# Kernel tuning notes

Measured on AMD Instinct MI355X. Metric: run time of the kernel, lower is better.

## Reference

```python
import jax, jax.numpy as jnp
import numpy as np

N, F, T, C = 20000, 4, 12, 256
HID, OUT = 128, 12
ER, E = 30000, 320000


def _gcn_agg(xw, src, dst, w):
    """GCNConv propagation with self-loops (weight 1): D^-1/2 (A+I) D^-1/2 @ xw.
    xw: [N, T, C] pre-projected features; src/dst: [E] int; w: [E] edge weights."""
    n = xw.shape[0]
    deg = jnp.zeros((n,), xw.dtype).at[dst].add(w) + 1.0  # +1 from self-loop
    dinv = jax.lax.rsqrt(deg)
    coef = (dinv[src] * w * dinv[dst])[:, None, None]      # [E,1,1]
    out = jnp.zeros_like(xw).at[dst].add(coef * xw[src])   # scatter-add messages
    return out + (dinv * dinv)[:, None, None] * xw         # self-loop term


def _regional_conv(x, Wc, bc, regs):
    # Shared GCNConv applied to each of the 5 state graphs, outputs summed.
    xw = jnp.einsum("nft,fc->ntc", x, Wc)  # [N, T, C], all periods at once
    out = bc
    for (src, dst, w) in regs:
        out = out + _gcn_agg(xw, src, dst, w)
    return out


def _forward(x, attrs, idxs, Wc_z, bc_z, Wl_z, bl_z, Wc_h, bc_h, Wl_h, bl_h,
             attention, W1, b1, W2, b2):
    regs = [(idx[0], idx[1], w) for idx, w in zip(idxs, attrs)]
    # A3TGCN runs an independent TGCN-GRU step per period from H=None (zeros),
    # then attention-averages over periods. With H=0:
    #   Z = sigmoid(linear_z([conv_z(X_t), 0]))   (hidden half of Wl drops out)
    #   reset gate R multiplies H=0, so it has no effect on the output
    #   H_tilde = tanh(linear_h([conv_h(X_t), 0]));  H_t = (1-Z)*H_tilde
    cz = _regional_conv(x, Wc_z, bc_z, regs)         # [N, T, C]
    Z = jax.nn.sigmoid(cz @ Wl_z[:C] + bl_z)
    ch = _regional_conv(x, Wc_h, bc_h, regs)
    Htilde = jnp.tanh(ch @ Wl_h[:C] + bl_h)
    Ht = (1.0 - Z) * Htilde                          # [N, T, C]
    probs = jax.nn.softmax(attention)                # [T]
    h = jnp.einsum("ntc,t->nc", Ht, probs)           # temporal attention pooling
    y = jax.nn.relu(h)
    y = jax.nn.relu(y @ W1 + b1)
    y = y @ W2 + b2
    return y, h


def setup_inputs():
    key = jax.random.key(0)
    ks = jax.random.split(key, 32)
    s = 0.05
    inp = {
        "x": jax.random.normal(ks[0], (N, F, T), jnp.float32),
        "edge_index": jax.random.randint(ks[1], (2, E), 0, N, jnp.int32),
    }
    regions = ["IA", "KS", "KY", "OH", "WI"]
    for i, nm in enumerate(regions):
        inp[nm + "edge_index"] = jax.random.randint(ks[2 + i], (2, ER), 0, N, jnp.int32)
    for i, nm in enumerate(regions):
        inp[nm + "edge_attr"] = jax.random.uniform(ks[7 + i], (ER,), jnp.float32)
    for gi, g in enumerate(["z", "r", "h"]):
        inp["Wc_" + g] = jax.random.normal(ks[12 + gi], (F, C), jnp.float32) * s
        inp["bc_" + g] = jnp.zeros((C,), jnp.float32)
        inp["Wl_" + g] = jax.random.normal(ks[15 + gi], (2 * C, C), jnp.float32) * s
        inp["bl_" + g] = jnp.zeros((C,), jnp.float32)
    inp["attention"] = jax.random.normal(ks[18], (T,), jnp.float32)
    inp["W1"] = jax.random.normal(ks[19], (C, HID), jnp.float32) * s
    inp["b1"] = jnp.zeros((HID,), jnp.float32)
    inp["W2"] = jax.random.normal(ks[20], (HID, OUT), jnp.float32) * s
    inp["b2"] = jnp.zeros((OUT,), jnp.float32)
    return inp


def reference(x, edge_index, IAedge_index, KSedge_index, KYedge_index, OHedge_index, WIedge_index,
              IAedge_attr, KSedge_attr, KYedge_attr, OHedge_attr, WIedge_attr,
              Wc_z, bc_z, Wl_z, bl_z, Wc_r, bc_r, Wl_r, bl_r, Wc_h, bc_h, Wl_h, bl_h,
              attention, W1, b1, W2, b2):
    # The full-graph edge_index and the reset-gate parameters are carried by the
    # original module but cannot influence the output (regional convs use the 5
    # state graphs; the reset gate multiplies the zero initial hidden state).
    idxs = [IAedge_index, KSedge_index, KYedge_index, OHedge_index, WIedge_index]
    attrs = [IAedge_attr, KSedge_attr, KYedge_attr, OHedge_attr, WIedge_attr]
    return _forward(x, attrs, idxs, Wc_z, bc_z, Wl_z, bl_z, Wc_h, bc_h, Wl_h, bl_h,
                    attention, W1, b1, W2, b2)
```

## Files before the change

### kernel.cpp

```cpp
#include <hip/hip_runtime.h>

constexpr int N    = 20000;
constexpr int T    = 12;
constexpr int C    = 256;
constexpr int HIDN = 128;
constexpr int OUTD = 12;
constexpr int ER   = 30000;
constexpr int NFT  = 48;
constexpr int EDGE_TOT = 5 * ER;
constexpr int CAP      = 32;
constexpr int EB       = 586;

constexpr int WS_DEG    = 0;
constexpr int WS_CNT    = 100000;
constexpr int WS_MV     = 120000;
constexpr int WS_ZEND   = 122576;
constexpr int WS_WP     = 122576;
constexpr int WS_W2T    = 138960;
constexpr int WS_XV     = 140496;
constexpr int WS_BUCKET = 1100496;

constexpr float LOG2E = 1.4426950408889634f;

typedef __attribute__((ext_vector_type(8))) short short8;
typedef __attribute__((ext_vector_type(4))) float floatx4;

#if __has_builtin(__builtin_amdgcn_exp2f)
#define EXP2(x) __builtin_amdgcn_exp2f(x)
#else
#define EXP2(x) exp2f(x)
#endif

__device__ __forceinline__ short f2bf(float f) {
  unsigned u = __float_as_uint(f);
  u = u + 0x7fffu + ((u >> 16) & 1u);
  return (short)(u >> 16);
}

__device__ __forceinline__ void pick_region(
    int r,
    const int* e0, const int* e1, const int* e2, const int* e3, const int* e4,
    const float* a0, const float* a1, const float* a2, const float* a3, const float* a4,
    const int*& ei, const float*& ea) {
  switch (r) {
    case 0: ei = e0; ea = a0; break;
    case 1: ei = e1; ea = a1; break;
    case 2: ei = e2; ea = a2; break;
    case 3: ei = e3; ea = a3; break;
    default: ei = e4; ea = a4; break;
  }
}

__global__ void k_prep_deg(
    const float* __restrict__ Wc_z, const float* __restrict__ bc_z,
    const float* __restrict__ Wl_z, const float* __restrict__ bl_z,
    const float* __restrict__ Wc_h, const float* __restrict__ bc_h,
    const float* __restrict__ Wl_h, const float* __restrict__ bl_h,
    const float* __restrict__ att, const float* __restrict__ W1,
    const float* __restrict__ W2,
    const int* __restrict__ e0, const int* __restrict__ e1,
    const int* __restrict__ e2, const int* __restrict__ e3,
    const int* __restrict__ e4,
    const float* __restrict__ a0, const float* __restrict__ a1,
    const float* __restrict__ a2, const float* __restrict__ a3,
    const float* __restrict__ a4,
    float* __restrict__ Mv, short* __restrict__ Wp, float* __restrict__ W2t,
    float* __restrict__ deg) {
  int b = blockIdx.x, tid = threadIdx.x;
  if (b < 16) {
    int g  = b >> 3;
    int ch = b & 7;
    int k  = tid;
    const float* Wc = g ? Wc_h : Wc_z;
    const float* bc = g ? bc_h : bc_z;
    const float* Wl = g ? Wl_h : Wl_z;
    const float* bl = g ? bl_h : bl_z;
    float scale = g ? 2.0f * LOG2E : LOG2E;
    float m0 = 0.f, m1 = 0.f, m2 = 0.f, m3 = 0.f;
    float v = (ch == 0) ? bl[k] : 0.0f;
    int c0 = ch * 32;
    for (int c = c0; c < c0 + 32; c++) {
      float wl = Wl[c * C + k];
      m0 = fmaf(Wc[0 * C + c], wl, m0);
      m1 = fmaf(Wc[1 * C + c], wl, m1);
      m2 = fmaf(Wc[2 * C + c], wl, m2);
      m3 = fmaf(Wc[3 * C + c], wl, m3);
      v  = fmaf(bc[c], wl, v);
    }
    float* o = Mv + g * (5 * C);
    atomicAdd(&o[0 * C + k], scale * m0);
    atomicAdd(&o[1 * C + k], scale * m1);
    atomicAdd(&o[2 * C + k], scale * m2);
    atomicAdd(&o[3 * C + k], scale * m3);
    atomicAdd(&o[4 * C + k], scale * v);
    return;
  }
  if (b == 16) {
    if (tid < T) {
      float amax = -3.0e38f;
      for (int t = 0; t < T; t++) amax = fmaxf(amax, att[t]);
      float s = 0.f;
      for (int t = 0; t < T; t++) s += __expf(att[t] - amax);
      Mv[10 * C + tid] = __expf(att[tid] - amax) / s;
    }
    return;
  }
  if (b < 152) {
    int idx = (b - 17) * 256 + tid;
    if (idx < 32768) {
      int j    = idx & 7;
      int lane = (idx >> 3) & 63;
      int ch   = (idx >> 9) & 7;
      int kt   = idx >> 12;
      int cin  = ch * 32 + (lane >> 4) * 8 + j;
      int kout = kt * 16 + (lane & 15);
      Wp[idx] = f2bf(W1[cin * HIDN + kout]);
    } else if (idx < 32768 + 1536) {
      int r = idx - 32768;
      int o = r >> 7, k = r & 127;
      W2t[r] = W2[k * OUTD + o];
    }
    return;
  }
  int i = (b - 152) * 256 + tid;
  if (i >= EDGE_TOT) return;
  int r = i / ER;
  int e = i - r * ER;
  const int* ei; const float* ea;
  pick_region(r, e0, e1, e2, e3, e4, a0, a1, a2, a3, a4, ei, ea);
  atomicAdd(&deg[r * N + ei[ER + e]], ea[e]);
}

__global__ void k_fill(const int* __restrict__ e0, const int* __restrict__ e1,
                       const int* __restrict__ e2, const int* __restrict__ e3,
                       const int* __restrict__ e4,
                       const float* __restrict__ a0, const float* __restrict__ a1,
                       const float* __restrict__ a2, const float* __restrict__ a3,
                       const float* __restrict__ a4,
                       const float* __restrict__ deg, int* __restrict__ cnt,
                       int2* __restrict__ bucket) {
  int i = blockIdx.x * blockDim.x + threadIdx.x;
  if (i >= EDGE_TOT) return;
  int r = i / ER;
  int e = i - r * ER;
  const int* ei; const float* ea;
  pick_region(r, e0, e1, e2, e3, e4, a0, a1, a2, a3, a4, ei, ea);
  int src = ei[e];
  int dst = ei[ER + e];
  float cf = rsqrtf(deg[r * N + src] + 1.0f) * ea[e] * rsqrtf(deg[r * N + dst] + 1.0f);
  int slot = atomicAdd(&cnt[dst], 1);
  if (slot < CAP) bucket[dst * CAP + slot] = make_int2(src, __float_as_int(cf));
}

__global__ __launch_bounds__(256) void k_gather(
    const float* __restrict__ x, const float* __restrict__ deg,
    const int* __restrict__ cnt, const int2* __restrict__ bucket,
    float* __restrict__ xv) {
  int wave = threadIdx.x >> 6, lane = threadIdx.x & 63;
  int n = blockIdx.x * 4 + wave;
  int q = lane < NFT ? lane : NFT - 1;
  float s = 0.f;
#pragma unroll
  for (int r = 0; r < 5; r++) s += 1.0f / (deg[r * N + n] + 1.0f);
  float facc = s * x[n * NFT + q];
  int cv = cnt[n];
  if (cv > CAP) cv = CAP;
  int2 mreg = bucket[n * CAP + (lane & (CAP - 1))];
  for (int j = 0; j < cv; j++) {
    int   src = __shfl(mreg.x, j);
    float cf  = __int_as_float(__shfl(mreg.y, j));
    facc = fmaf(cf, x[src * NFT + q], facc);
  }
  if (lane < NFT) xv[n * NFT + q] = facc;
}

__global__ __launch_bounds__(256) void k_gates(
    const float* __restrict__ xv, const float* __restrict__ Mv,
    float* __restrict__ h_out) {
  int wave = threadIdx.x >> 6, lane = threadIdx.x & 63;
  int n = blockIdx.x * 2 + (wave >> 1);
  int half = wave & 1;
  int c0 = half * 128 + (lane << 1);
  const float* Mz = Mv;
  const float* Mh = Mv + 5 * C;
  float mz[4][2], mh[4][2], vz[2], vh[2];
#pragma unroll
  for (int f = 0; f < 4; f++) {
    float2 t1 = *(const float2*)(Mz + f * C + c0);
    mz[f][0] = t1.x; mz[f][1] = t1.y;
    float2 t2 = *(const float2*)(Mh + f * C + c0);
    mh[f][0] = t2.x; mh[f][1] = t2.y;
  }
  {
    float2 t1 = *(const float2*)(Mz + 4 * C + c0);
    vz[0] = t1.x; vz[1] = t1.y;
    float2 t2 = *(const float2*)(Mh + 4 * C + c0);
    vh[0] = t2.x; vh[1] = t2.y;
  }

  const float* xr = xv + n * NFT;
  float acc[2] = {0.f, 0.f};
#pragma unroll
  for (int tb = 0; tb < 3; tb++) {
    float4 xf0 = *(const float4*)(xr + 0 * T + tb * 4);
    float4 xf1 = *(const float4*)(xr + 1 * T + tb * 4);
    float4 xf2 = *(const float4*)(xr + 2 * T + tb * 4);
    float4 xf3 = *(const float4*)(xr + 3 * T + tb * 4);
    float xs0[4] = {xf0.x, xf0.y, xf0.z, xf0.w};
    float xs1[4] = {xf1.x, xf1.y, xf1.z, xf1.w};
    float xs2[4] = {xf2.x, xf2.y, xf2.z, xf2.w};
    float xs3[4] = {xf3.x, xf3.y, xf3.z, xf3.w};
#pragma unroll
    for (int tt = 0; tt < 4; tt++) {
      int t = tb * 4 + tt;
      float p = Mv[10 * C + t];
      float x0 = xs0[tt], x1 = xs1[tt], x2 = xs2[tt], x3 = xs3[tt];
#pragma unroll
      for (int j = 0; j < 2; j++) {
        float az = fmaf(mz[0][j], x0, fmaf(mz[1][j], x1, fmaf(mz[2][j], x2, fmaf(mz[3][j], x3, vz[j]))));
        float ah = fmaf(mh[0][j], x0, fmaf(mh[1][j], x1, fmaf(mh[2][j], x2, fmaf(mh[3][j], x3, vh[j]))));
        float e1 = EXP2(az);
        float e2 = EXP2(ah);
        float den = (1.0f + e1) * (1.0f + e2);
        float rD  = __builtin_amdgcn_rcpf(den);
        float pn  = fmaf(p, e2, -p);
        acc[j] = fmaf(pn, rD, acc[j]);
      }
    }
  }
  float2 o = {acc[0], acc[1]};
  *(float2*)(h_out + n * C + c0) = o;
}

__global__ __launch_bounds__(256) void k_mlp16(
    const float* __restrict__ h_in, const short* __restrict__ Wp,
    const float* __restrict__ b1, const float* __restrict__ W2t,
    const float* __restrict__ b2, float* __restrict__ y_out) {
  __shared__ short hs[16][264];
  __shared__ float y1s[16][132];
  int tid = threadIdx.x;
  int wave = tid >> 6, lane = tid & 63;
  int quad = lane >> 4, col = lane & 15;
  int n0 = blockIdx.x * 16;
  int c0 = lane << 2;

#pragma unroll
  for (int nl = 0; nl < 4; nl++) {
    int rl = wave * 4 + nl;
    float4 hv = *(const float4*)(h_in + (n0 + rl) * C + c0);
    unsigned lo = (unsigned short)f2bf(fmaxf(hv.x, 0.f)) |
                  ((unsigned)(unsigned short)f2bf(fmaxf(hv.y, 0.f)) << 16);
    unsigned hi = (unsigned short)f2bf(fmaxf(hv.z, 0.f)) |
                  ((unsigned)(unsigned short)f2bf(fmaxf(hv.w, 0.f)) << 16);
    *(int2*)&hs[rl][c0] = make_int2((int)lo, (int)hi);
  }
  __syncthreads();

  floatx4 acc2[2];
  acc2[0] = {0.f, 0.f, 0.f, 0.f};
  acc2[1] = {0.f, 0.f, 0.f, 0.f};
#pragma unroll
  for (int ch = 0; ch < 8; ch++) {
    short8 a = *(const short8*)&hs[col][ch * 32 + quad * 8];
#pragma unroll
    for (int kk = 0; kk < 2; kk++) {
      short8 b = ((const short8*)Wp)[((wave * 2 + kk) * 8 + ch) * 64 + lane];
      acc2[kk] = __builtin_amdgcn_mfma_f32_16x16x32_bf16(a, b, acc2[kk], 0, 0, 0);
    }
  }
#pragma unroll
  for (int kk = 0; kk < 2; kk++) {
    int kt = wave * 2 + kk;
    float bias = b1[kt * 16 + col];
#pragma unroll
    for (int r = 0; r < 4; r++)
      y1s[quad * 4 + r][kt * 16 + col] = fmaxf(acc2[kk][r] + bias, 0.f);
  }
  __syncthreads();

  if (tid < 16 * OUTD) {
    int nl = tid / OUTD, o = tid - nl * OUTD;
    float sacc = b2[o];
    const float* yr = &y1s[nl][0];
    const float* wr = W2t + o * HIDN;
#pragma unroll 8
    for (int k4 = 0; k4 < 32; k4++) {
      float4 yv = *(const float4*)(yr + 4 * k4);
      float4 wv = *(const float4*)(wr + 4 * k4);
      sacc = fmaf(yv.x, wv.x, fmaf(yv.y, wv.y, fmaf(yv.z, wv.z, fmaf(yv.w, wv.w, sacc))));
    }
    y_out[(n0 + nl) * OUTD + o] = sacc;
  }
}

extern "C" void kernel_launch(void* const* d_in, const int* in_sizes, int n_in,
                              void* d_out, int out_size, void* d_ws, size_t ws_size,
                              hipStream_t stream) {
  const float* x   = (const float*)d_in[0];
  const int* eIA = (const int*)d_in[2];
  const int* eKS = (const int*)d_in[3];
  const int* eKY = (const int*)d_in[4];
  const int* eOH = (const int*)d_in[5];
  const int* eWI = (const int*)d_in[6];
  const float* aIA = (const float*)d_in[7];
  const float* aKS = (const float*)d_in[8];
  const float* aKY = (const float*)d_in[9];
  const float* aOH = (const float*)d_in[10];
  const float* aWI = (const float*)d_in[11];
  const float* Wc_z = (const float*)d_in[12];
  const float* bc_z = (const float*)d_in[13];
  const float* Wl_z = (const float*)d_in[14];
  const float* bl_z = (const float*)d_in[15];
  const float* Wc_h = (const float*)d_in[20];
  const float* bc_h = (const float*)d_in[21];
  const float* Wl_h = (const float*)d_in[22];
  const float* bl_h = (const float*)d_in[23];
  const float* att  = (const float*)d_in[24];
  const float* W1   = (const float*)d_in[25];
  const float* b1   = (const float*)d_in[26];
  const float* W2   = (const float*)d_in[27];
  const float* b2   = (const float*)d_in[28];

  float* ws     = (float*)d_ws;
  float* deg    = ws + WS_DEG;
  int*   cnt    = (int*)(ws + WS_CNT);
  float* Mv     = ws + WS_MV;
  short* Wp     = (short*)(ws + WS_WP);
  float* W2t    = ws + WS_W2T;
  float* xvb    = ws + WS_XV;
  int2*  bucket = (int2*)(ws + WS_BUCKET);

  float* y_out = (float*)d_out;
  float* h_out = y_out + N * OUTD;

  hipMemsetAsync(deg, 0, WS_ZEND * sizeof(float), stream);

  k_prep_deg<<<152 + EB, 256, 0, stream>>>(Wc_z, bc_z, Wl_z, bl_z,
                                           Wc_h, bc_h, Wl_h, bl_h,
                                           att, W1, W2,
                                           eIA, eKS, eKY, eOH, eWI,
                                           aIA, aKS, aKY, aOH, aWI,
                                           Mv, Wp, W2t, deg);
  k_fill<<<EB, 256, 0, stream>>>(eIA, eKS, eKY, eOH, eWI,
                                 aIA, aKS, aKY, aOH, aWI,
                                 deg, cnt, bucket);
  k_gather<<<N / 4, 256, 0, stream>>>(x, deg, cnt, bucket, xvb);
  k_gates<<<N / 2, 256, 0, stream>>>(xvb, Mv, h_out);
  k_mlp16<<<N / 16, 256, 0, stream>>>(h_out, Wp, b1, W2t, b2, y_out);
}
```

Baseline: 212.4 us.

## Fuse gate computation and MLP head into a single kernel

Merges the gating kernel and the bf16 MFMA MLP kernel so each 16-node block computes the gated, attention-pooled hidden state and writes its relu'd bf16 form directly into shared memory for the MLP. This removes one kernel launch and the global re-read of h. The trade-off is fewer blocks (N/16 instead of N/2), with each wave now processing 8 nodes serially, which reduces parallelism for the transcendental-heavy gate work. A launch-bounds occupancy hint is also added.

New measurement: 277.1 us. +30.5%, slower.

```diff
diff --git a/kernel.cpp b/kernel.cpp
--- a/kernel.cpp
+++ b/kernel.cpp
@@ -174,85 +174,77 @@
   if (lane < NFT) xv[n * NFT + q] = facc;
 }
 
-__global__ __launch_bounds__(256) void k_gates(
+__global__ __launch_bounds__(256, 6) void k_gates_mlp(
     const float* __restrict__ xv, const float* __restrict__ Mv,
-    float* __restrict__ h_out) {
-  int wave = threadIdx.x >> 6, lane = threadIdx.x & 63;
-  int n = blockIdx.x * 2 + (wave >> 1);
-  int half = wave & 1;
-  int c0 = half * 128 + (lane << 1);
-  const float* Mz = Mv;
-  const float* Mh = Mv + 5 * C;
-  float mz[4][2], mh[4][2], vz[2], vh[2];
-#pragma unroll
-  for (int f = 0; f < 4; f++) {
-    float2 t1 = *(const float2*)(Mz + f * C + c0);
-    mz[f][0] = t1.x; mz[f][1] = t1.y;
-    float2 t2 = *(const float2*)(Mh + f * C + c0);
-    mh[f][0] = t2.x; mh[f][1] = t2.y;
-  }
-  {
-    float2 t1 = *(const float2*)(Mz + 4 * C + c0);
-    vz[0] = t1.x; vz[1] = t1.y;
-    float2 t2 = *(const float2*)(Mh + 4 * C + c0);
-    vh[0] = t2.x; vh[1] = t2.y;
-  }
-
-  const float* xr = xv + n * NFT;
-  float acc[2] = {0.f, 0.f};
-#pragma unroll
-  for (int tb = 0; tb < 3; tb++) {
-    float4 xf0 = *(const float4*)(xr + 0 * T + tb * 4);
-    float4 xf1 = *(const float4*)(xr + 1 * T + tb * 4);
-    float4 xf2 = *(const float4*)(xr + 2 * T + tb * 4);
-    float4 xf3 = *(const float4*)(xr + 3 * T + tb * 4);
-    float xs0[4] = {xf0.x, xf0.y, xf0.z, xf0.w};
-    float xs1[4] = {xf1.x, xf1.y, xf1.z, xf1.w};
-    float xs2[4] = {xf2.x, xf2.y, xf2.z, xf2.w};
-    float xs3[4] = {xf3.x, xf3.y, xf3.z, xf3.w};
-#pragma unroll
-    for (int tt = 0; tt < 4; tt++) {
-      int t = tb * 4 + tt;
-      float p = Mv[10 * C + t];
-      float x0 = xs0[tt], x1 = xs1[tt], x2 = xs2[tt], x3 = xs3[tt];
-#pragma unroll
-      for (int j = 0; j < 2; j++) {
-        float az = fmaf(mz[0][j], x0, fmaf(mz[1][j], x1, fmaf(mz[2][j], x2, fmaf(mz[3][j], x3, vz[j]))));
-        float ah = fmaf(mh[0][j], x0, fmaf(mh[1][j], x1, fmaf(mh[2][j], x2, fmaf(mh[3][j], x3, vh[j]))));
-        float e1 = EXP2(az);
-        float e2 = EXP2(ah);
-        float den = (1.0f + e1) * (1.0f + e2);
-        float rD  = __builtin_amdgcn_rcpf(den);
-        float pn  = fmaf(p, e2, -p);
-        acc[j] = fmaf(pn, rD, acc[j]);
-      }
-    }
-  }
-  float2 o = {acc[0], acc[1]};
-  *(float2*)(h_out + n * C + c0) = o;
-}
-
-__global__ __launch_bounds__(256) void k_mlp16(
-    const float* __restrict__ h_in, const short* __restrict__ Wp,
-    const float* __restrict__ b1, const float* __restrict__ W2t,
-    const float* __restrict__ b2, float* __restrict__ y_out) {
+    const short* __restrict__ Wp, const float* __restrict__ b1,
+    const float* __restrict__ W2t, const float* __restrict__ b2,
+    float* __restrict__ y_out, float* __restrict__ h_out) {
   __shared__ short hs[16][264];
   __shared__ float y1s[16][132];
   int tid = threadIdx.x;
   int wave = tid >> 6, lane = tid & 63;
   int quad = lane >> 4, col = lane & 15;
   int n0 = blockIdx.x * 16;
-  int c0 = lane << 2;
-
-#pragma unroll
-  for (int nl = 0; nl < 4; nl++) {
-    int rl = wave * 4 + nl;
-    float4 hv = *(const float4*)(h_in + (n0 + rl) * C + c0);
-    unsigned lo = (unsigned short)f2bf(fmaxf(hv.x, 0.f)) |
-                  ((unsigned)(unsigned short)f2bf(fmaxf(hv.y, 0.f)) << 16);
-    unsigned hi = (unsigned short)f2bf(fmaxf(hv.z, 0.f)) |
-                  ((unsigned)(unsigned short)f2bf(fmaxf(hv.w, 0.f)) << 16);
-    *(int2*)&hs[rl][c0] = make_int2((int)lo, (int)hi);
+
+  int half = wave & 1;
+  int nb   = (wave >> 1) * 8;
+  int c0 = half * 128 + (lane << 1);
+  const float* Mz = Mv;
+  const float* Mh = Mv + 5 * C;
+  float mz[4][2], mh[4][2], vz[2], vh[2];
+#pragma unroll
+  for (int f = 0; f < 4; f++) {
+    float2 t1 = *(const float2*)(Mz + f * C + c0);
+    mz[f][0] = t1.x; mz[f][1] = t1.y;
+    float2 t2 = *(const float2*)(Mh + f * C + c0);
+    mh[f][0] = t2.x; mh[f][1] = t2.y;
+  }
+  {
+    float2 t1 = *(const float2*)(Mz + 4 * C + c0);
+    vz[0] = t1.x; vz[1] = t1.y;
+    float2 t2 = *(const float2*)(Mh + 4 * C + c0);
+    vh[0] = t2.x; vh[1] = t2.y;
+  }
+
+#pragma unroll
+  for (int nl = 0; nl < 8; nl++) {
+    int rl = nb + nl;
+    int n = n0 + rl;
+    const float* xr = xv + n * NFT;
+    float acc[2] = {0.f, 0.f};
+#pragma unroll
+    for (int tb = 0; tb < 3; tb++) {
+      float4 xf0 = *(const float4*)(xr + 0 * T + tb * 4);
+      float4 xf1 = *(const float4*)(xr + 1 * T + tb * 4);
+      float4 xf2 = *(const float4*)(xr + 2 * T + tb * 4);
+      float4 xf3 = *(const float4*)(xr + 3 * T + tb * 4);
+      float xs0[4] = {xf0.x, xf0.y, xf0.z, xf0.w};
+      float xs1[4] = {xf1.x, xf1.y, xf1.z, xf1.w};
+      float xs2[4] = {xf2.x, xf2.y, xf2.z, xf2.w};
+      float xs3[4] = {xf3.x, xf3.y, xf3.z, xf3.w};
+#pragma unroll
+      for (int tt = 0; tt < 4; tt++) {
+        int t = tb * 4 + tt;
+        float p = Mv[10 * C + t];
+        float x0 = xs0[tt], x1 = xs1[tt], x2 = xs2[tt], x3 = xs3[tt];
+#pragma unroll
+        for (int j = 0; j < 2; j++) {
+          float az = fmaf(mz[0][j], x0, fmaf(mz[1][j], x1, fmaf(mz[2][j], x2, fmaf(mz[3][j], x3, vz[j]))));
+          float ah = fmaf(mh[0][j], x0, fmaf(mh[1][j], x1, fmaf(mh[2][j], x2, fmaf(mh[3][j], x3, vh[j]))));
+          float e1 = EXP2(az);
+          float e2 = EXP2(ah);
+          float den = (1.0f + e1) * (1.0f + e2);
+          float rD  = __builtin_amdgcn_rcpf(den);
+          float pn  = fmaf(p, e2, -p);
+          acc[j] = fmaf(pn, rD, acc[j]);
+        }
+      }
+    }
+    float2 o = {acc[0], acc[1]};
+    *(float2*)(h_out + n * C + c0) = o;
+    unsigned pk = (unsigned short)f2bf(fmaxf(acc[0], 0.f)) |
+                  ((unsigned)(unsigned short)f2bf(fmaxf(acc[1], 0.f)) << 16);
+    *(unsigned*)&hs[rl][c0] = pk;
   }
   __syncthreads();
 
@@ -345,6 +337,5 @@
                                  aIA, aKS, aKY, aOH, aWI,
                                  deg, cnt, bucket);
   k_gather<<<N / 4, 256, 0, stream>>>(x, deg, cnt, bucket, xvb);
-  k_gates<<<N / 2, 256, 0, stream>>>(xvb, Mv, h_out);
-  k_mlp16<<<N / 16, 256, 0, stream>>>(h_out, Wp, b1, W2t, b2, y_out);
-}
+  k_gates_mlp<<<N / 16, 256, 0, stream>>>(xvb, Mv, Wp, b1, W2t, b2, y_out, h_out);
+}
```
